# Kernel optimization log

Measured on AMD Instinct MI355X. Metric: run time of the kernel, lower is better.

Reference implementation:

```python
import jax, jax.numpy as jnp
import numpy as np

B = 32
D = 64

def _ragged_layout():
    b = np.arange(B)
    q_len = 64 + 4 * b              # ragged query lengths per batch element
    k_len = 64 + 4 * (B - 1 - b)    # ragged key lengths per batch element
    q_off = np.concatenate([[0], np.cumsum(q_len)])  # row splits for queries
    k_off = np.concatenate([[0], np.cumsum(k_len)])
    q_pair, k_pair = [], []
    for i in range(B):
        # all (query, key) pairs within batch element i (what the nested
        # value_rowids gathers in _mul_broadcast_ragged produce)
        q_pair.append(q_off[i] + np.repeat(np.arange(q_len[i]), k_len[i]))
        k_pair.append(k_off[i] + np.tile(np.arange(k_len[i]), q_len[i]))
    return (int(q_off[-1]), int(k_off[-1]),
            np.concatenate(q_pair).astype(np.int64),
            np.concatenate(k_pair).astype(np.int64))

def setup_inputs() -> dict:
    key = jax.random.key(0)
    kq, kk = jax.random.split(key)
    n_q, n_k, q_pair_idx, k_pair_idx = _ragged_layout()
    queries = jax.random.normal(kq, (n_q, D), dtype=jnp.float32)  # flat ragged values
    keys = jax.random.normal(kk, (n_k, D), dtype=jnp.float32)
    return {
        "queries": queries,
        "keys": keys,
        "q_pair_idx": jnp.asarray(q_pair_idx),
        "k_pair_idx": jnp.asarray(k_pair_idx),
    }

def reference(queries, keys, q_pair_idx, k_pair_idx):
    # broadcast_ragged: gather both sides to the flat pair dimension, then
    # per-pair dot product ('ij,ij->i'). Output is the flat values of the
    # [B,(q_i),(k_i)] ragged logits tensor.
    q = queries[q_pair_idx]  # [P, D]
    k = keys[k_pair_idx]     # [P, D]
    return jnp.einsum('pd,pd->p', q, k)
```

## Files before the change

### kernel.cpp

```cpp
#include <hip/hip_runtime.h>


#define TILE 16
#define LDS_STRIDE 68

__global__ __launch_bounds__(256) void qk_ragged_dot(
    const float* __restrict__ q,
    const float* __restrict__ k,
    float* __restrict__ out)
{
    const int i = blockIdx.y;
    const int q_len = 64 + 4 * i;
    const int k_len = 188 - 4 * i;
    const int tq = (q_len + TILE - 1) >> 4;
    const int tk = (k_len + TILE - 1) >> 4;
    const int tile = blockIdx.x;
    if (tile >= tq * tk) return;
    const int qt = tile / tk;
    const int kt = tile % tk;

    const long q_off = 64L * i + 2L * i * (i - 1);
    const long k_off = 188L * i - 2L * i * (i - 1);
    const long s2 = (long)(i - 1) * i * (2 * i - 1) / 6;
    const long pair_off = 12032L * i + 248L * i * (i - 1) - 16L * s2;

    __shared__ float qs[TILE][LDS_STRIDE];
    __shared__ float ks[TILE][LDS_STRIDE];

    const int tid = threadIdx.x;

    {
        const int row = tid >> 4;
        const int c4  = tid & 15;
        int qr = qt * TILE + row; if (qr > q_len - 1) qr = q_len - 1;
        int kr = kt * TILE + row; if (kr > k_len - 1) kr = k_len - 1;
        *(float4*)&qs[row][c4 * 4] =
            *(const float4*)&q[(q_off + qr) * 64 + c4 * 4];
        *(float4*)&ks[row][c4 * 4] =
            *(const float4*)&k[(k_off + kr) * 64 + c4 * 4];
    }
    __syncthreads();

    const int ty = tid >> 4;
    const int tx = tid & 15;
    float acc = 0.0f;
    #pragma unroll
    for (int j = 0; j < 16; ++j) {
        const float4 a = *(const float4*)&qs[ty][j * 4];
        const float4 b = *(const float4*)&ks[tx][j * 4];
        acc += a.x * b.x + a.y * b.y + a.z * b.z + a.w * b.w;
    }

    const int r = qt * TILE + ty;
    const int c = kt * TILE + tx;
    if (r < q_len && c < k_len)
        out[pair_off + (long)r * k_len + c] = acc;
}

extern "C" void kernel_launch(void* const* d_in, const int* in_sizes, int n_in,
                              void* d_out, int out_size, void* d_ws, size_t ws_size,
                              hipStream_t stream) {
    const float* q = (const float*)d_in[0];
    const float* k = (const float*)d_in[1];
    float* out = (float*)d_out;

    dim3 grid(72, 32, 1);
    dim3 block(256, 1, 1);
    qk_ragged_dot<<<grid, block, 0, stream>>>(q, k, out);
}
```

Measured before the change: 11.58 us.

## Compute ragged QK dot tiles with bf16 MFMA on 64x64 block tiles

Replaces the scalar FP32 16x16 tile dot product with 64x64 tiles, where the inputs are converted to bf16 in LDS and multiplied with mfma_f32_16x16x32_bf16 across four waves. The grid shrinks from 72 to 6 tiles per batch element. This cuts per-block overhead and redundant input loads, and moves the arithmetic onto matrix cores. Rounding inputs to bf16 loses precision against the FP32 reference, which could break tolerance checks. Output stores now go column-strided per lane, which is less coalesced.

After: 10.04 us. 1.15x faster.

```diff
diff --git a/kernel.cpp b/kernel.cpp
--- a/kernel.cpp
+++ b/kernel.cpp
@@ -1,10 +1,18 @@
 #include <hip/hip_runtime.h>
 
 
-#define TILE 16
-#define LDS_STRIDE 68
+typedef __attribute__((ext_vector_type(8))) short short8;
+typedef __attribute__((ext_vector_type(4))) float float4v;
 
-__global__ __launch_bounds__(256) void qk_ragged_dot(
+#define LDSS 72
+
+__device__ __forceinline__ ushort f2bf_rne(float f) {
+    unsigned u = __float_as_uint(f);
+    u += 0x7FFFu + ((u >> 16) & 1u);
+    return (ushort)(u >> 16);
+}
+
+__global__ __launch_bounds__(256) void qk_ragged_mfma(
     const float* __restrict__ q,
     const float* __restrict__ k,
     float* __restrict__ out)
@@ -12,8 +20,8 @@
     const int i = blockIdx.y;
     const int q_len = 64 + 4 * i;
     const int k_len = 188 - 4 * i;
-    const int tq = (q_len + TILE - 1) >> 4;
-    const int tk = (k_len + TILE - 1) >> 4;
+    const int tq = (q_len + 63) >> 6;
+    const int tk = (k_len + 63) >> 6;
     const int tile = blockIdx.x;
     if (tile >= tq * tk) return;
     const int qt = tile / tk;
@@ -24,37 +32,74 @@
     const long s2 = (long)(i - 1) * i * (2 * i - 1) / 6;
     const long pair_off = 12032L * i + 248L * i * (i - 1) - 16L * s2;
 
-    __shared__ float qs[TILE][LDS_STRIDE];
-    __shared__ float ks[TILE][LDS_STRIDE];
+    __shared__ ushort Qs[64][LDSS];
+    __shared__ ushort Ks[64][LDSS];
 
-    const int tid = threadIdx.x;
+    const int t = threadIdx.x;
 
     {
-        const int row = tid >> 4;
-        const int c4  = tid & 15;
-        int qr = qt * TILE + row; if (qr > q_len - 1) qr = q_len - 1;
-        int kr = kt * TILE + row; if (kr > k_len - 1) kr = k_len - 1;
-        *(float4*)&qs[row][c4 * 4] =
-            *(const float4*)&q[(q_off + qr) * 64 + c4 * 4];
-        *(float4*)&ks[row][c4 * 4] =
-            *(const float4*)&k[(k_off + kr) * 64 + c4 * 4];
+        const int row = t >> 2;
+        const int quad = t & 3;
+        int qr = qt * 64 + row; if (qr > q_len - 1) qr = q_len - 1;
+        int kr = kt * 64 + row; if (kr > k_len - 1) kr = k_len - 1;
+        const float* qrow = q + (q_off + qr) * 64;
+        const float* krow = k + (k_off + kr) * 64;
+        #pragma unroll
+        for (int c = 0; c < 4; ++c) {
+            const int f4 = quad + 4 * c;
+            float4 a = *(const float4*)(qrow + 4 * f4);
+            float4 b = *(const float4*)(krow + 4 * f4);
+            ushort4 ua = make_ushort4(f2bf_rne(a.x), f2bf_rne(a.y),
+                                      f2bf_rne(a.z), f2bf_rne(a.w));
+            ushort4 ub = make_ushort4(f2bf_rne(b.x), f2bf_rne(b.y),
+                                      f2bf_rne(b.z), f2bf_rne(b.w));
+            *(ushort4*)&Qs[row][4 * f4] = ua;
+            *(ushort4*)&Ks[row][4 * f4] = ub;
+        }
     }
     __syncthreads();
 
-    const int ty = tid >> 4;
-    const int tx = tid & 15;
-    float acc = 0.0f;
+    const int lane = t & 63;
+    const int wave = t >> 6;
+    const int wr = wave >> 1;
+    const int wc = wave & 1;
+    const int fr = lane & 15;
+    const int fh = lane >> 4;
+
+    short8 a[2][2], b[2][2];
     #pragma unroll
-    for (int j = 0; j < 16; ++j) {
-        const float4 a = *(const float4*)&qs[ty][j * 4];
-        const float4 b = *(const float4*)&ks[tx][j * 4];
-        acc += a.x * b.x + a.y * b.y + a.z * b.z + a.w * b.w;
+    for (int s = 0; s < 2; ++s)
+        #pragma unroll
+        for (int kh = 0; kh < 2; ++kh) {
+            a[s][kh] = *(const short8*)&Qs[wr * 32 + s * 16 + fr][kh * 32 + fh * 8];
+            b[s][kh] = *(const short8*)&Ks[wc * 32 + s * 16 + fr][kh * 32 + fh * 8];
+        }
+
+    float4v acc[2][2] = {};
+    #pragma unroll
+    for (int si = 0; si < 2; ++si)
+        #pragma unroll
+        for (int sj = 0; sj < 2; ++sj)
+            #pragma unroll
+            for (int kh = 0; kh < 2; ++kh)
+                acc[si][sj] = __builtin_amdgcn_mfma_f32_16x16x32_bf16(
+                    a[si][kh], b[sj][kh], acc[si][sj], 0, 0, 0);
+
+    #pragma unroll
+    for (int si = 0; si < 2; ++si) {
+        #pragma unroll
+        for (int sj = 0; sj < 2; ++sj) {
+            const int c = kt * 64 + wc * 32 + sj * 16 + fr;
+            if (c < k_len) {
+                #pragma unroll
+                for (int j = 0; j < 4; ++j) {
+                    const int r = qt * 64 + wr * 32 + si * 16 + fh * 4 + j;
+                    if (r < q_len)
+                        out[pair_off + (long)r * k_len + c] = acc[si][sj][j];
+                }
+            }
+        }
     }
-
-    const int r = qt * TILE + ty;
-    const int c = kt * TILE + tx;
-    if (r < q_len && c < k_len)
-        out[pair_off + (long)r * k_len + c] = acc;
 }
 
 extern "C" void kernel_launch(void* const* d_in, const int* in_sizes, int n_in,
@@ -64,7 +109,7 @@
     const float* k = (const float*)d_in[1];
     float* out = (float*)d_out;
 
-    dim3 grid(72, 32, 1);
+    dim3 grid(6, 32, 1);
     dim3 block(256, 1, 1);
-    qk_ragged_dot<<<grid, block, 0, stream>>>(q, k, out);
+    qk_ragged_mfma<<<grid, block, 0, stream>>>(q, k, out);
 }
```
